# Optimization experiments

Measured on AMD Instinct MI355X. Metric: run time of the kernel, lower is better.

Reference implementation:

```python
import jax, jax.numpy as jnp
import numpy as np

H = 300  # hidden size hardcoded in the module
VX = 32000
VY = 32000
NX, NY, B = 128, 128, 256


def setup_inputs() -> dict:
    key = jax.random.key(0)
    ks = jax.random.split(key, 10)
    s = 1.0 / np.sqrt(H)
    x = jax.random.randint(ks[0], (NX, B), 0, VX)
    y = jax.random.randint(ks[1], (NY, B), 0, VY)
    # padding_idx=0: zero the pad row of each embedding table
    enc_emb = jax.random.normal(ks[2], (VX, H), jnp.float32).at[0].set(0.0)
    encW = jax.random.uniform(ks[3], (H, H), jnp.float32, -s, s)
    encb = jax.random.uniform(ks[4], (H,), jnp.float32, -s, s)
    dec_emb = jax.random.normal(ks[5], (VY, H), jnp.float32).at[0].set(0.0)
    decW = jax.random.uniform(ks[6], (H, H), jnp.float32, -s, s)
    decb = jax.random.uniform(ks[7], (H,), jnp.float32, -s, s)
    outW = jax.random.uniform(ks[8], (VY, H), jnp.float32, -s, s)
    outb = jax.random.uniform(ks[9], (VY,), jnp.float32, -s, s)
    return {"x": x, "y": y, "enc_emb": enc_emb, "encW": encW, "encb": encb,
            "dec_emb": dec_emb, "decW": decW, "decb": decb,
            "outW": outW, "outb": outb}


def reference(x, y, enc_emb, encW, encb, dec_emb, decW, decb, outW, outb):
    # Encoder: Elman recurrence h = relu(e_x[i] + W h + b)
    e_x = enc_emb[x]                                  # [NX, B, H]
    h0 = jnp.zeros((x.shape[1], H), e_x.dtype)        # h=0 broadcast over batch

    def enc_step(h, ex):
        return jax.nn.relu(ex + h @ encW.T + encb), None

    h, _ = jax.lax.scan(enc_step, h0, e_x)

    # Decoder: teacher-forced recurrence with per-step mean cross-entropy
    e_y = dec_emb[y]                                  # [NY, B, H]

    def dec_step(h, inp):
        ey, tgt = inp
        h = jax.nn.relu(ey + h @ decW.T + decb)
        logits = h @ outW.T + outb                    # [B, VY]
        logp = jax.nn.log_softmax(logits, axis=-1)
        ce = -jnp.mean(jnp.take_along_axis(logp, tgt[:, None], axis=-1))
        return h, ce

    _, ces = jax.lax.scan(dec_step, h, (e_y[:-1], y[1:]))
    return jnp.sum(ces)
```

## Files before the change

kernel.cpp:

```cpp
#include <hip/hip_runtime.h>
#include <hip/hip_bf16.h>
#include <stdint.h>

typedef unsigned short u16;
typedef unsigned char u8;
typedef float f32x4 __attribute__((ext_vector_type(4)));
typedef float f32x2 __attribute__((ext_vector_type(2)));
typedef _Float16 f16x2 __attribute__((ext_vector_type(2)));
typedef _Float16 f16x8 __attribute__((ext_vector_type(8)));

#define H      300
#define KP     320
#define BATCH  256
#define NX     128
#define NY     128
#define VY     32000
#define NPAD   32768
#define MROWS  32512

#define OW8_OFF  0UL
#define OW8_BYTES ((unsigned long)NPAD * KP)
#define A8_OFF   (OW8_OFF + OW8_BYTES)
#define A8_BYTES ((unsigned long)MROWS * KP)
#define WTE_OFF  (A8_OFF + A8_BYTES)
#define WT_BYTES ((unsigned long)H * KP * 4)
#define WTD_OFF  (WTE_OFF + WT_BYTES)
#define SE_OFF   (WTD_OFF + WT_BYTES)
#define SE_BYTES ((unsigned long)MROWS * 4)

typedef const __attribute__((address_space(1))) char* gp_t;
typedef __attribute__((address_space(3))) char* lp_t;

__global__ __launch_bounds__(256) void k0_prep(const float* __restrict__ outW,
                                               const float* __restrict__ encW,
                                               const float* __restrict__ decW,
                                               u8* __restrict__ ow8,
                                               float* __restrict__ wte,
                                               float* __restrict__ wtd) {
    long id = (long)blockIdx.x * 256 + threadIdx.x;
    const long n1 = (long)NPAD * KP / 4;
    if (id < n1) {
        int v = (int)(id / 80), k4 = (int)(id % 80) * 4;
        float4 f = {0.f, 0.f, 0.f, 0.f};
        if (v < VY && k4 < H) f = *(const float4*)&outW[(long)v * H + k4];
        int w = __builtin_amdgcn_cvt_pk_fp8_f32(f.x, f.y, 0, false);
        w = __builtin_amdgcn_cvt_pk_fp8_f32(f.z, f.w, w, true);
        ((unsigned int*)ow8)[id] = (unsigned int)w;
        return;
    }
    long id2 = id - n1;
    if (id2 < (long)H * KP) {
        int k = (int)(id2 / KP), j = (int)(id2 % KP);
        wte[id2] = (j < H) ? encW[j * H + k] : 0.f;
        return;
    }
    id2 -= (long)H * KP;
    if (id2 < (long)H * KP) {
        int k = (int)(id2 / KP), j = (int)(id2 % KP);
        wtd[id2] = (j < H) ? decW[j * H + k] : 0.f;
    }
}

__global__ __launch_bounds__(960, 4) void k1_rnn(const int* __restrict__ x,
                                                 const int* __restrict__ y,
                                                 const float* __restrict__ enc_emb,
                                                 const float* __restrict__ dec_emb,
                                                 const float* __restrict__ encb,
                                                 const float* __restrict__ decb,
                                                 const float* __restrict__ wte,
                                                 const float* __restrict__ wtd,
                                                 u8* __restrict__ A8) {
    const int tid = threadIdx.x;
    const int s = tid / 320;
    const int j = tid - s * 320;
    const int b = blockIdx.x;

    __shared__ __align__(16) _Float16 hh[320];
    __shared__ float part[960];

    for (int i = tid; i < 320; i += 960) hh[i] = (_Float16)0.f;

    const bool comb = (tid < 320);
    const float be = (comb && j < H) ? encb[j] : 0.f;
    const float bd = (comb && j < H) ? decb[j] : 0.f;

    f16x2 w[52];
#pragma unroll
    for (int kk = 0; kk < 52; ++kk) {
        int k0 = 2 * (s * 52 + kk);
        float f0 = (k0 < H)     ? wte[k0 * KP + j]       : 0.f;
        float f1 = (k0 + 1 < H) ? wte[(k0 + 1) * KP + j] : 0.f;
        w[kk] = (f16x2){(_Float16)f0, (_Float16)f1};
    }

    int idx_n = x[BATCH + b];
    float e_cur = 0.f;
    if (comb && j < H) e_cur = enc_emb[(long)x[b] * H + j];
    __syncthreads();

    const f16x8* hb8 = (const f16x8*)&hh[s * 104];

    for (int t = 0; t < NX; ++t) {
        int idx_n2 = x[min(t + 2, NX - 1) * BATCH + b];
        float e_nx = 0.f;
        if (comb && j < H && t + 1 < NX) e_nx = enc_emb[(long)idx_n * H + j];

        float p0 = 0.f, p1 = 0.f;
#pragma unroll
        for (int i = 0; i < 13; ++i) {
            f16x8 hv = hb8[i];
            f16x2 a0 = {hv[0], hv[1]}, a1 = {hv[2], hv[3]};
            f16x2 a2 = {hv[4], hv[5]}, a3 = {hv[6], hv[7]};
            p0 = __builtin_amdgcn_fdot2(w[4 * i + 0], a0, p0, false);
            p1 = __builtin_amdgcn_fdot2(w[4 * i + 1], a1, p1, false);
            p0 = __builtin_amdgcn_fdot2(w[4 * i + 2], a2, p0, false);
            p1 = __builtin_amdgcn_fdot2(w[4 * i + 3], a3, p1, false);
        }
        part[tid] = p0 + p1;
        __syncthreads();
        if (comb) {
            float v = part[j] + part[320 + j] + part[640 + j] + be + e_cur;
            hh[j] = (_Float16)fmaxf(v, 0.f);
        }
        __syncthreads();
        e_cur = e_nx; idx_n = idx_n2;
    }

#pragma unroll
    for (int kk = 0; kk < 52; ++kk) {
        int k0 = 2 * (s * 52 + kk);
        float f0 = (k0 < H)     ? wtd[k0 * KP + j]       : 0.f;
        float f1 = (k0 + 1 < H) ? wtd[(k0 + 1) * KP + j] : 0.f;
        w[kk] = (f16x2){(_Float16)f0, (_Float16)f1};
    }

    idx_n = y[BATCH + b];
    e_cur = 0.f;
    if (comb && j < H) e_cur = dec_emb[(long)y[b] * H + j];

    for (int t = 0; t < NY - 1; ++t) {
        int idx_n2 = y[min(t + 2, NY - 1) * BATCH + b];
        float e_nx = 0.f;
        if (comb && j < H && t + 1 < NY - 1) e_nx = dec_emb[(long)idx_n * H + j];

        float p0 = 0.f, p1 = 0.f;
#pragma unroll
        for (int i = 0; i < 13; ++i) {
            f16x8 hv = hb8[i];
            f16x2 a0 = {hv[0], hv[1]}, a1 = {hv[2], hv[3]};
            f16x2 a2 = {hv[4], hv[5]}, a3 = {hv[6], hv[7]};
            p0 = __builtin_amdgcn_fdot2(w[4 * i + 0], a0, p0, false);
            p1 = __builtin_amdgcn_fdot2(w[4 * i + 1], a1, p1, false);
            p0 = __builtin_amdgcn_fdot2(w[4 * i + 2], a2, p0, false);
            p1 = __builtin_amdgcn_fdot2(w[4 * i + 3], a3, p1, false);
        }
        part[tid] = p0 + p1;
        __syncthreads();
        if (comb) {
            float v = part[j] + part[320 + j] + part[640 + j] + bd + e_cur;
            v = fmaxf(v, 0.f);
            hh[j] = (_Float16)v;
            int pk = __builtin_amdgcn_cvt_pk_fp8_f32(v, v, 0, false);
            A8[(long)(t * BATCH + b) * KP + j] = (u8)(pk & 0xff);
        }
        __syncthreads();
        e_cur = e_nx; idx_n = idx_n2;
    }
}

__global__ __launch_bounds__(512, 4) void k2_gemm(const u8* __restrict__ A8,
                                                  const u8* __restrict__ OW8,
                                                  const float* __restrict__ outb,
                                                  float* __restrict__ sumexp) {
    const int tid = threadIdx.x;
    const int lane = tid & 63, wave = tid >> 6;
    const int lane16 = lane & 15, quad = lane >> 4;
    const int wr = wave >> 2, wc = wave & 3;
    const int cg = blockIdx.x & 7;
    const int rb = blockIdx.x >> 3;

    __shared__ u8 Ald[128 * 336];
    __shared__ u8 Bld[2][8192];
    __shared__ float rowsum[128];
    if (tid < 128) rowsum[tid] = 0.f;

    {
        const u8* ag = A8 + (long)rb * 128 * KP;
#pragma unroll
        for (int i = 0; i < 5; ++i) {
            int t2 = i * 512 + tid;
            int row = t2 / 20, o = t2 % 20;
            uint4 v = *(const uint4*)(ag + row * 320 + o * 16);
            *(uint4*)&Ald[row * 336 + o * 16] = v;
        }
    }

    const int colbase = cg * 4096;

    auto stage = [&](int it, int buf) {
        int ct = it / 10, ks = it - ct * 10;
        int v0 = colbase + ct * 256;
        int col = tid >> 1, kq = tid & 1;
        const u8* g = OW8 + (long)(v0 + col) * KP + ks * 32 + kq * 16;
        u8* l = &Bld[buf][0] + tid * 16;
        __builtin_amdgcn_global_load_lds((gp_t)g, (lp_t)l, 16, 0, 0);
    };

    f32x4 acc[4][4];
    float rsum[16];
#pragma unroll
    for (int s = 0; s < 16; ++s) rsum[s] = 0.f;

    stage(0, 0);
    for (int it = 0; it < 160; ++it) {
        int ct = it / 10, ks = it - ct * 10;
        __syncthreads();
        if (it + 1 < 160) stage(it + 1, (it + 1) & 1);
        if (ks == 0) {
#pragma unroll
            for (int a = 0; a < 4; ++a)
#pragma unroll
                for (int b = 0; b < 4; ++b) acc[a][b] = (f32x4){0.f, 0.f, 0.f, 0.f};
        }
        const u8* Bb = &Bld[it & 1][0];
        long af[4], bfr[4];
#pragma unroll
        for (int tr = 0; tr < 4; ++tr)
            af[tr] = *(const long*)&Ald[(wr * 64 + tr * 16 + lane16) * 336 + ks * 32 + quad * 8];
#pragma unroll
        for (int tc = 0; tc < 4; ++tc) {
            int col = wc * 64 + tc * 16 + lane16;
            bfr[tc] = *(const long*)&Bb[col * 32 + quad * 8];
        }
#pragma unroll
        for (int tr = 0; tr < 4; ++tr)
#pragma unroll
            for (int tc = 0; tc < 4; ++tc)
                acc[tr][tc] = __builtin_amdgcn_mfma_f32_16x16x32_fp8_fp8(af[tr], bfr[tc], acc[tr][tc], 0, 0, 0);

        if (ks == 9) {
            int cb = colbase + ct * 256 + wc * 64;
#pragma unroll
            for (int tc = 0; tc < 4; ++tc) {
                int v = cb + tc * 16 + lane16;
                bool valid = v < VY;
                float ob = valid ? outb[v] : 0.f;
#pragma unroll
                for (int tr = 0; tr < 4; ++tr)
#pragma unroll
                    for (int i = 0; i < 4; ++i) {
                        float lg = acc[tr][tc][i] + ob;
                        if (valid) rsum[tr * 4 + i] += __expf(lg);
                    }
            }
        }
    }

#pragma unroll
    for (int m = 1; m < 16; m <<= 1)
#pragma unroll
        for (int s = 0; s < 16; ++s) rsum[s] += __shfl_xor(rsum[s], m, 64);
    if (lane16 == 0) {
#pragma unroll
        for (int tr = 0; tr < 4; ++tr)
#pragma unroll
            for (int i = 0; i < 4; ++i)
                atomicAdd(&rowsum[wr * 64 + tr * 16 + quad * 4 + i], rsum[tr * 4 + i]);
    }
    __syncthreads();
    if (tid < 128) atomicAdd(&sumexp[(long)rb * 128 + tid], rowsum[tid]);
}

__global__ __launch_bounds__(256) void k3_ce(const u8* __restrict__ A8,
                                             const u8* __restrict__ OW8,
                                             const float* __restrict__ outb,
                                             const float* __restrict__ sumexp,
                                             const int* __restrict__ y,
                                             float* __restrict__ out) {
    const int wave = threadIdx.x >> 6, lane = threadIdx.x & 63;
    const int r = blockIdx.x * 4 + wave;
    const int t = r >> 8, b = r & 255;
    const int tgt = y[(t + 1) * BATCH + b];
    const unsigned int* ar = (const unsigned int*)(A8 + (long)r * KP);
    const unsigned int* wr_ = (const unsigned int*)(OW8 + (long)tgt * KP);
    float s = 0.f;
#pragma unroll
    for (int i = 0; i < 2; ++i) {
        int c = i * 64 + lane;
        if (c < 80) {
            unsigned int a4 = ar[c], w4 = wr_[c];
            f32x2 al = __builtin_amdgcn_cvt_pk_f32_fp8(a4, false);
            f32x2 ah = __builtin_amdgcn_cvt_pk_f32_fp8(a4, true);
            f32x2 wl = __builtin_amdgcn_cvt_pk_f32_fp8(w4, false);
            f32x2 wh = __builtin_amdgcn_cvt_pk_f32_fp8(w4, true);
            s += al[0] * wl[0] + al[1] * wl[1] + ah[0] * wh[0] + ah[1] * wh[1];
        }
    }
#pragma unroll
    for (int m = 1; m < 64; m <<= 1) s += __shfl_xor(s, m, 64);
    __shared__ float part[4];
    if (lane == 0) part[wave] = logf(sumexp[r]) - (s + outb[tgt]);
    __syncthreads();
    if (threadIdx.x == 0) {
        float tot = part[0] + part[1] + part[2] + part[3];
        atomicAdd(out, tot * (1.0f / 256.0f));
    }
}

extern "C" void kernel_launch(void* const* d_in, const int* in_sizes, int n_in,
                              void* d_out, int out_size, void* d_ws, size_t ws_size,
                              hipStream_t stream) {
    (void)in_sizes; (void)n_in; (void)out_size; (void)ws_size;
    const int*   x       = (const int*)d_in[0];
    const int*   y       = (const int*)d_in[1];
    const float* enc_emb = (const float*)d_in[2];
    const float* encW    = (const float*)d_in[3];
    const float* encb    = (const float*)d_in[4];
    const float* dec_emb = (const float*)d_in[5];
    const float* decW    = (const float*)d_in[6];
    const float* decb    = (const float*)d_in[7];
    const float* outW    = (const float*)d_in[8];
    const float* outb    = (const float*)d_in[9];

    char* ws = (char*)d_ws;
    u8* ow8  = (u8*)(ws + OW8_OFF);
    u8* A8   = (u8*)(ws + A8_OFF);
    float* wte    = (float*)(ws + WTE_OFF);
    float* wtd    = (float*)(ws + WTD_OFF);
    float* sumexp = (float*)(ws + SE_OFF);

    hipMemsetAsync(sumexp, 0, SE_BYTES, stream);
    hipMemsetAsync(d_out, 0, sizeof(float), stream);

    long n0 = (long)NPAD * KP / 4 + 2L * H * KP;
    k0_prep<<<(int)((n0 + 255) / 256), 256, 0, stream>>>(outW, encW, decW, ow8, wte, wtd);
    k1_rnn<<<256, 960, 0, stream>>>(x, y, enc_emb, dec_emb, encb, decb, wte, wtd, A8);
    k2_gemm<<<254 * 8, 512, 0, stream>>>(A8, ow8, outb, sumexp);
    k3_ce<<<8128, 256, 0, stream>>>(A8, ow8, outb, sumexp, y, (float*)d_out);
}
```

Before: 1.153 ms.

## Restructure vocab GEMM to register-resident A tiles with per-wave B pipelining

The logits GEMM now uses 256-thread blocks covering 64 rows. Each wave keeps its whole A fragment (64 rows by K=320) in registers and streams its own B columns through a private 4-slot LDS ring with vmcnt waits, so block-wide barriers in the main loop are gone. The RNN kernel also stages each fp8 hidden row in shared memory and writes it out as 80 dword stores instead of 320 byte stores. The GEMM change raises register pressure and halves A reuse per B tile, which doubles total B traffic from global memory.

```diff
diff --git a/kernel.cpp b/kernel.cpp
--- a/kernel.cpp
+++ b/kernel.cpp
@@ -77,6 +77,7 @@
 
     __shared__ __align__(16) _Float16 hh[320];
     __shared__ float part[960];
+    __shared__ __align__(4) u8 a8row[320];
 
     for (int i = tid; i < 320; i += 960) hh[i] = (_Float16)0.f;
 
@@ -161,114 +162,116 @@
             v = fmaxf(v, 0.f);
             hh[j] = (_Float16)v;
             int pk = __builtin_amdgcn_cvt_pk_fp8_f32(v, v, 0, false);
-            A8[(long)(t * BATCH + b) * KP + j] = (u8)(pk & 0xff);
+            a8row[j] = (u8)(pk & 0xff);
         }
         __syncthreads();
+        if (tid < 80)
+            ((unsigned int*)(A8 + (long)(t * BATCH + b) * KP))[tid] =
+                ((const unsigned int*)a8row)[tid];
         e_cur = e_nx; idx_n = idx_n2;
     }
 }
 
-__global__ __launch_bounds__(512, 4) void k2_gemm(const u8* __restrict__ A8,
+__global__ __launch_bounds__(256, 2) void k2_gemm(const u8* __restrict__ A8,
                                                   const u8* __restrict__ OW8,
                                                   const float* __restrict__ outb,
                                                   float* __restrict__ sumexp) {
     const int tid = threadIdx.x;
     const int lane = tid & 63, wave = tid >> 6;
     const int lane16 = lane & 15, quad = lane >> 4;
-    const int wr = wave >> 2, wc = wave & 3;
     const int cg = blockIdx.x & 7;
     const int rb = blockIdx.x >> 3;
-
-    __shared__ u8 Ald[128 * 336];
-    __shared__ u8 Bld[2][8192];
-    __shared__ float rowsum[128];
-    if (tid < 128) rowsum[tid] = 0.f;
-
+    const int colbase = cg * 4096;
+
+    __shared__ u8 Bld[4 * 8192];
+    __shared__ float rowsum[64];
+    if (tid < 64) rowsum[tid] = 0.f;
+    __syncthreads();
+
+    u8* wbuf = &Bld[wave * 8192];
+
+    long a[4][10];
     {
-        const u8* ag = A8 + (long)rb * 128 * KP;
-#pragma unroll
-        for (int i = 0; i < 5; ++i) {
-            int t2 = i * 512 + tid;
-            int row = t2 / 20, o = t2 % 20;
-            uint4 v = *(const uint4*)(ag + row * 320 + o * 16);
-            *(uint4*)&Ald[row * 336 + o * 16] = v;
-        }
-    }
-
-    const int colbase = cg * 4096;
-
-    auto stage = [&](int it, int buf) {
-        int ct = it / 10, ks = it - ct * 10;
-        int v0 = colbase + ct * 256;
-        int col = tid >> 1, kq = tid & 1;
-        const u8* g = OW8 + (long)(v0 + col) * KP + ks * 32 + kq * 16;
-        u8* l = &Bld[buf][0] + tid * 16;
-        __builtin_amdgcn_global_load_lds((gp_t)g, (lp_t)l, 16, 0, 0);
+        const u8* abase = A8 + ((long)rb * 64 + lane16) * KP + quad * 8;
+#pragma unroll
+        for (int rt = 0; rt < 4; ++rt)
+#pragma unroll
+            for (int ks = 0; ks < 10; ++ks)
+                a[rt][ks] = *(const long*)(abase + rt * 16 * KP + ks * 32);
+    }
+
+    auto stage = [&](int ct3, int ks3, int slot) {
+        int colb = colbase + ct3 * 256 + wave * 64;
+        const u8* g0 = OW8 + (long)(colb + (lane >> 1)) * KP + ks3 * 32 + (lane & 1) * 16;
+        u8* l0 = wbuf + slot * 2048 + lane * 16;
+        __builtin_amdgcn_global_load_lds((gp_t)g0, (lp_t)l0, 16, 0, 0);
+        __builtin_amdgcn_global_load_lds((gp_t)(g0 + 32 * KP), (lp_t)(l0 + 1024), 16, 0, 0);
     };
 
-    f32x4 acc[4][4];
+    stage(0, 0, 0); stage(0, 1, 1); stage(0, 2, 2);
+
     float rsum[16];
 #pragma unroll
-    for (int s = 0; s < 16; ++s) rsum[s] = 0.f;
-
-    stage(0, 0);
-    for (int it = 0; it < 160; ++it) {
-        int ct = it / 10, ks = it - ct * 10;
-        __syncthreads();
-        if (it + 1 < 160) stage(it + 1, (it + 1) & 1);
-        if (ks == 0) {
-#pragma unroll
-            for (int a = 0; a < 4; ++a)
-#pragma unroll
-                for (int b = 0; b < 4; ++b) acc[a][b] = (f32x4){0.f, 0.f, 0.f, 0.f};
-        }
-        const u8* Bb = &Bld[it & 1][0];
-        long af[4], bfr[4];
-#pragma unroll
-        for (int tr = 0; tr < 4; ++tr)
-            af[tr] = *(const long*)&Ald[(wr * 64 + tr * 16 + lane16) * 336 + ks * 32 + quad * 8];
+    for (int i = 0; i < 16; ++i) rsum[i] = 0.f;
+
+    for (int ct = 0; ct < 16; ++ct) {
+        f32x4 acc[4][4];
+#pragma unroll
+        for (int p = 0; p < 4; ++p)
+#pragma unroll
+            for (int q = 0; q < 4; ++q) acc[p][q] = (f32x4){0.f, 0.f, 0.f, 0.f};
+
+#pragma unroll
+        for (int ks = 0; ks < 10; ++ks) {
+            int s_ct = (ks + 3 < 10) ? ct : ct + 1;
+            int s_ks = (ks + 3 < 10) ? (ks + 3) : (ks - 7);
+            if (s_ct > 15) { s_ct = 15; s_ks = 9; }
+            stage(s_ct, s_ks, (ct * 10 + ks + 3) & 3);
+
+            __builtin_amdgcn_s_waitcnt(0x0F76);
+
+            const u8* rb8 = wbuf + ((ct * 10 + ks) & 3) * 2048;
+            long bfr[4];
+#pragma unroll
+            for (int tc = 0; tc < 4; ++tc)
+                bfr[tc] = *(const long*)&rb8[(tc * 16 + lane16) * 32 + quad * 8];
+#pragma unroll
+            for (int rt = 0; rt < 4; ++rt)
+#pragma unroll
+                for (int tc = 0; tc < 4; ++tc)
+                    acc[rt][tc] = __builtin_amdgcn_mfma_f32_16x16x32_fp8_fp8(
+                        a[rt][ks], bfr[tc], acc[rt][tc], 0, 0, 0);
+        }
+
+        int cb = colbase + ct * 256 + wave * 64;
 #pragma unroll
         for (int tc = 0; tc < 4; ++tc) {
-            int col = wc * 64 + tc * 16 + lane16;
-            bfr[tc] = *(const long*)&Bb[col * 32 + quad * 8];
-        }
-#pragma unroll
-        for (int tr = 0; tr < 4; ++tr)
-#pragma unroll
-            for (int tc = 0; tc < 4; ++tc)
-                acc[tr][tc] = __builtin_amdgcn_mfma_f32_16x16x32_fp8_fp8(af[tr], bfr[tc], acc[tr][tc], 0, 0, 0);
-
-        if (ks == 9) {
-            int cb = colbase + ct * 256 + wc * 64;
-#pragma unroll
-            for (int tc = 0; tc < 4; ++tc) {
-                int v = cb + tc * 16 + lane16;
-                bool valid = v < VY;
-                float ob = valid ? outb[v] : 0.f;
-#pragma unroll
-                for (int tr = 0; tr < 4; ++tr)
-#pragma unroll
-                    for (int i = 0; i < 4; ++i) {
-                        float lg = acc[tr][tc][i] + ob;
-                        if (valid) rsum[tr * 4 + i] += __expf(lg);
-                    }
-            }
+            int v = cb + tc * 16 + lane16;
+            bool valid = v < VY;
+            float ob = valid ? outb[v] : 0.f;
+#pragma unroll
+            for (int rt = 0; rt < 4; ++rt)
+#pragma unroll
+                for (int i = 0; i < 4; ++i) {
+                    float lg = acc[rt][tc][i] + ob;
+                    if (valid) rsum[rt * 4 + i] += __expf(lg);
+                }
         }
     }
 
 #pragma unroll
     for (int m = 1; m < 16; m <<= 1)
 #pragma unroll
-        for (int s = 0; s < 16; ++s) rsum[s] += __shfl_xor(rsum[s], m, 64);
+        for (int i = 0; i < 16; ++i) rsum[i] += __shfl_xor(rsum[i], m, 64);
     if (lane16 == 0) {
 #pragma unroll
-        for (int tr = 0; tr < 4; ++tr)
+        for (int rt = 0; rt < 4; ++rt)
 #pragma unroll
             for (int i = 0; i < 4; ++i)
-                atomicAdd(&rowsum[wr * 64 + tr * 16 + quad * 4 + i], rsum[tr * 4 + i]);
+                atomicAdd(&rowsum[rt * 16 + quad * 4 + i], rsum[rt * 4 + i]);
     }
     __syncthreads();
-    if (tid < 128) atomicAdd(&sumexp[(long)rb * 128 + tid], rowsum[tid]);
+    if (tid < 64) atomicAdd(&sumexp[(long)rb * 64 + tid], rowsum[tid]);
 }
 
 __global__ __launch_bounds__(256) void k3_ce(const u8* __restrict__ A8,
@@ -335,6 +338,6 @@
     long n0 = (long)NPAD * KP / 4 + 2L * H * KP;
     k0_prep<<<(int)((n0 + 255) / 256), 256, 0, stream>>>(outW, encW, decW, ow8, wte, wtd);
     k1_rnn<<<256, 960, 0, stream>>>(x, y, enc_emb, dec_emb, encb, decb, wte, wtd, A8);
-    k2_gemm<<<254 * 8, 512, 0, stream>>>(A8, ow8, outb, sumexp);
+    k2_gemm<<<508 * 8, 256, 0, stream>>>(A8, ow8, outb, sumexp);
     k3_ce<<<8128, 256, 0, stream>>>(A8, ow8, outb, sumexp, y, (float*)d_out);
 }
```

After: 1.193 ms. 3.5% more time.
